# Kernel tuning notes

Hardware: AMD Instinct MI355X
Metric: run time of the kernel (lower is better)

Reference implementation:

```python
import jax, jax.numpy as jnp
import numpy as np

B, C, H, W, S = 4, 16, 256, 256, 100
OMEGA2 = (0.01 * S) ** 2  # alpha=0.01, n_spixels=100 -> 1.0
EPS = 1e-32


def setup_inputs() -> dict:
    key = jax.random.key(0)
    ks = jax.random.split(key, 7)
    pf = jax.random.normal(ks[0], (B, C, H, W), jnp.float32)
    spf1 = jax.random.normal(ks[1], (B, C, S), jnp.float32)
    spf2 = jax.random.normal(ks[2], (B, C, S), jnp.float32)
    Q1 = jax.random.uniform(ks[3], (B, S, H * W), jnp.float32)
    Q2 = jax.random.uniform(ks[4], (B, S, H * W), jnp.float32)
    w_ds = jax.random.normal(ks[5], (2, C, 3, 3), jnp.float32) * 0.05
    b_ds = jnp.zeros((2,), jnp.float32)
    return {"pf": pf, "spf1": spf1, "spf2": spf2, "Q1": Q1, "Q2": Q2,
            "w_ds": w_ds, "b_ds": b_ds}


def _affinity_pool(pf_flat, spf, Q):
    """merge=True branch: pairwise superpixel affinities, then affinity-weighted
    normalized pixel->superpixel pooling.
    pf_flat: [B,C,N], spf: [B,C,S] (detached), Q: [B,S,N] (detached)."""
    d = spf[:, :, None, :] - spf[:, :, :, None]          # [B,C,S,S]
    rels = jnp.exp(-jnp.sum(d * d, axis=1) / OMEGA2)      # [B,S,S]
    coeffs = jnp.einsum('bst,btn->bsn', rels, Q)          # map_sp2p(rels, Q)
    num = jnp.einsum('bcn,bsn->bcs', pf_flat, coeffs)     # pf @ coeffs^T
    return num / (jnp.sum(coeffs, axis=-1)[:, None, :] + EPS)  # [B,C,S]


def reference(pf, spf1, spf2, Q1, Q2, w_ds, b_ds):
    b, c, h, w = pf.shape
    pf_flat = pf.reshape(b, c, h * w)
    spf1n = _affinity_pool(pf_flat, spf1, Q1)
    spf2n = _affinity_pool(pf_flat, spf2, Q2)
    # map_sp2p: superpixel features back to pixels
    pf1 = jnp.einsum('bcs,bsn->bcn', spf1n, Q1).reshape(b, c, h, w)
    pf2 = jnp.einsum('bcs,bsn->bcn', spf2n, Q2).reshape(b, c, h, w)
    pf_sp = pf1 + pf2
    # conv_ds: Conv3x3(out_ch, 2), no bn/act
    prob_ds = jax.lax.conv_general_dilated(
        pf_sp, w_ds, window_strides=(1, 1), padding='SAME',
        dimension_numbers=('NCHW', 'OIHW', 'NCHW')) + b_ds[None, :, None, None]
    return prob_ds
```

## Files before the change

kernel.cpp:

```cpp
#include <hip/hip_runtime.h>

#define BB 4
#define CC 16
#define HH 256
#define WW 256
#define NN (HH*WW)
#define SS 100
#define SPL 5
#define EPSV 1e-32f

#define PQ_OFF    0u
#define SPFN_OFF  217600u
#define PFSP_OFF  230400u
#define PPART_OFF PFSP_OFF

__device__ __forceinline__ float dot4(const float4& a, const float4& b) {
    return a.x * b.x + a.y * b.y + a.z * b.z + a.w * b.w;
}
__device__ __forceinline__ void fma2g(float2& a, float c1, const float2& v1,
                                      float c2, const float2& v2) {
    a.x += c1 * v1.x + c2 * v2.x;
    a.y += c1 * v1.y + c2 * v2.y;
}

#define DPPQP(x, ctrl) __int_as_float(__builtin_amdgcn_update_dpp( \
    0, __float_as_int(x), ctrl, 0xF, 0xF, true))

__device__ __forceinline__ float dpp_sum64(float x) {
    #define DPPADD(ctrl) \
        x += __int_as_float(__builtin_amdgcn_update_dpp( \
            0, __float_as_int(x), ctrl, 0xF, 0xF, true));
    DPPADD(0x111)
    DPPADD(0x112)
    DPPADD(0x114)
    DPPADD(0x118)
    DPPADD(0x142)
    DPPADD(0x143)
    #undef DPPADD
    return x;
}

#define P1_LD0(k) (*(const float4*)(qptr + (size_t)(k) * NN))
#define P1_LD1(k) (*(const float4*)(qptr + (size_t)(k) * NN + 256))

#define P1_STEP(Q0, Q1, sidx) { \
    float t0 = dot4(p00,Q0)+dot4(p01,Q1), t1 = dot4(p10,Q0)+dot4(p11,Q1); \
    float t2 = dot4(p20,Q0)+dot4(p21,Q1), t3 = dot4(p30,Q0)+dot4(p31,Q1); \
    float t4 = dot4(p40,Q0)+dot4(p41,Q1), t5 = dot4(p50,Q0)+dot4(p51,Q1); \
    float t6 = dot4(p60,Q0)+dot4(p61,Q1), t7 = dot4(p70,Q0)+dot4(p71,Q1); \
    t0 += DPPQP(t0,0xB1); t1 += DPPQP(t1,0xB1); \
    t2 += DPPQP(t2,0xB1); t3 += DPPQP(t3,0xB1); \
    t4 += DPPQP(t4,0xB1); t5 += DPPQP(t5,0xB1); \
    t6 += DPPQP(t6,0xB1); t7 += DPPQP(t7,0xB1); \
    float u0 = odd ? t1 : t0; float u1 = odd ? t3 : t2; \
    float u2 = odd ? t5 : t4; float u3 = odd ? t7 : t6; \
    u0 += DPPQP(u0,0x4E); u1 += DPPQP(u1,0x4E); \
    u2 += DPPQP(u2,0x4E); u3 += DPPQP(u3,0x4E); \
    float w0 = hi2 ? u1 : u0; float w1 = hi2 ? u3 : u2; \
    w0 += DPPQP(w0,0x114); w1 += DPPQP(w1,0x114); \
    w0 += DPPQP(w0,0x118); w1 += DPPQP(w1,0x118); \
    w0 += __shfl_xor(w0,16); w1 += __shfl_xor(w1,16); \
    w0 += __shfl_xor(w0,32); w1 += __shfl_xor(w1,32); \
    float qv = Q0.x+Q0.y+Q0.z+Q0.w + Q1.x+Q1.y+Q1.z+Q1.w; \
    qv = dpp_sum64(qv); \
    if (h == 0 && lane == 63) sout[(size_t)(sidx)*17 + 16] = qv; \
    if (lane >= 12 && lane < 16) { \
        float* o = sout + (size_t)(sidx)*17 + h*8 + (lane-12); \
        o[0] = w0; o[4] = w1; \
    } \
}

__global__ __launch_bounds__(256, 4) void k_pass1(const float* __restrict__ pf,
                                                  const float* __restrict__ Q1,
                                                  const float* __restrict__ Q2,
                                                  float* __restrict__ ws) {
    int tid = threadIdx.x, wid = tid >> 6, lane = tid & 63;
    int h  = wid & 1;
    int nh = wid >> 1;
    int win = blockIdx.x;
    int sp  = blockIdx.y;
    int bq  = blockIdx.z;
    int b = bq >> 1, q = bq & 1;
    bool odd = lane & 1;
    bool hi2 = lane & 2;

    int nbase = win * 1024 + nh * 512 + lane * 4;
    const float* qptr = (q ? Q2 : Q1) + (size_t)b * SS * NN
                        + (size_t)(sp * 20) * NN + nbase;
    const float* PF   = pf + (size_t)b * CC * NN + (size_t)(h * 8) * NN + nbase;

    float4 p00 = *(const float4*)(PF + (size_t)0 * NN);
    float4 p01 = *(const float4*)(PF + (size_t)0 * NN + 256);
    float4 p10 = *(const float4*)(PF + (size_t)1 * NN);
    float4 p11 = *(const float4*)(PF + (size_t)1 * NN + 256);
    float4 p20 = *(const float4*)(PF + (size_t)2 * NN);
    float4 p21 = *(const float4*)(PF + (size_t)2 * NN + 256);
    float4 p30 = *(const float4*)(PF + (size_t)3 * NN);
    float4 p31 = *(const float4*)(PF + (size_t)3 * NN + 256);
    float4 p40 = *(const float4*)(PF + (size_t)4 * NN);
    float4 p41 = *(const float4*)(PF + (size_t)4 * NN + 256);
    float4 p50 = *(const float4*)(PF + (size_t)5 * NN);
    float4 p51 = *(const float4*)(PF + (size_t)5 * NN + 256);
    float4 p60 = *(const float4*)(PF + (size_t)6 * NN);
    float4 p61 = *(const float4*)(PF + (size_t)6 * NN + 256);
    float4 p70 = *(const float4*)(PF + (size_t)7 * NN);
    float4 p71 = *(const float4*)(PF + (size_t)7 * NN + 256);

    float* sout = ws + PPART_OFF
                + (size_t)((((bq * 64 + win) * 2 + nh) * SPL) + sp) * (20 * 17);

    float4 A0 = P1_LD0(0), A1 = P1_LD1(0), B0, B1;
    for (int s = 0; s < 17; s += 2) {
        B0 = P1_LD0(s + 1); B1 = P1_LD1(s + 1);
        P1_STEP(A0, A1, s)
        A0 = P1_LD0(s + 2); A1 = P1_LD1(s + 2);
        P1_STEP(B0, B1, s + 1)
    }
    B0 = P1_LD0(19); B1 = P1_LD1(19);
    P1_STEP(A0, A1, 18)
    P1_STEP(B0, B1, 19)
}

__global__ __launch_bounds__(256) void k_reduceP(float* __restrict__ ws) {
    int wg = blockIdx.x;
    int bq = blockIdx.y;
    int tid = threadIdx.x;
    const float* pp = ws + PPART_OFF + (size_t)(bq * 128 + wg * 16) * 1700;
    float a0 = 0.f, a1 = 0.f, a2 = 0.f, a3 = 0.f, a4 = 0.f, a5 = 0.f, a6 = 0.f;
    for (int wv = 0; wv < 16; ++wv) {
        const float* p = pp + (size_t)wv * 1700;
        a0 += p[tid];
        a1 += p[256 + tid];
        a2 += p[512 + tid];
        a3 += p[768 + tid];
        a4 += p[1024 + tid];
        a5 += p[1280 + tid];
        a6 += (1536 + tid < 1700) ? p[1536 + tid] : 0.f;
    }
    float* o = ws + PQ_OFF + (size_t)(bq * 8 + wg) * 1700;
    o[tid] = a0; o[256 + tid] = a1; o[512 + tid] = a2; o[768 + tid] = a3;
    o[1024 + tid] = a4; o[1280 + tid] = a5;
    if (1536 + tid < 1700) o[1536 + tid] = a6;
}

__global__ __launch_bounds__(256) void k_finalize(const float* __restrict__ spf1,
                                                  const float* __restrict__ spf2,
                                                  float* __restrict__ ws) {
    int bq = blockIdx.x;
    int b = bq >> 1, q = bq & 1;
    __shared__ float sp[CC][SS];
    __shared__ float rl[SS][SS + 1];
    __shared__ float Pl[CC * SS];
    __shared__ float qs[SS];
    __shared__ float den[SS];
    int tid = threadIdx.x;

    const float* spf = (q ? spf2 : spf1) + (size_t)b * CC * SS;
    for (int i = tid; i < CC * SS; i += 256) sp[i / SS][i % SS] = spf[i];
    __syncthreads();
    for (int i = tid; i < SS * SS; i += 256) {
        int s = i / SS, t = i % SS;
        float d2 = 0.f;
        #pragma unroll
        for (int c = 0; c < CC; ++c) {
            float d = sp[c][t] - sp[c][s];
            d2 += d * d;
        }
        rl[s][t] = expf(-d2);
    }
    const float* pq = ws + PQ_OFF + (size_t)bq * 8 * 1700;
    for (int idx = tid; idx < CC * SS; idx += 256) {
        int c = idx / SS, s = idx % SS;
        int slot = (s / 20) * 340 + (s % 20) * 17 + c;
        float v = 0.f;
        #pragma unroll 4
        for (int g = 0; g < 8; ++g) v += pq[(size_t)g * 1700 + slot];
        Pl[idx] = v;
    }
    if (tid < SS) {
        int slot = (tid / 20) * 340 + (tid % 20) * 17 + 16;
        float v = 0.f;
        #pragma unroll 4
        for (int g = 0; g < 8; ++g) v += pq[(size_t)g * 1700 + slot];
        qs[tid] = v;
    }
    __syncthreads();
    if (tid < SS) {
        float a = 0.f;
        for (int t = 0; t < SS; ++t) a += rl[tid][t] * qs[t];
        den[tid] = a + EPSV;
    }
    __syncthreads();
    float* sout = ws + SPFN_OFF + (size_t)bq * CC * SS;
    for (int idx = tid; idx < CC * SS; idx += 256) {
        int c = idx / SS, s = idx % SS;
        float a = 0.f;
        for (int t = 0; t < SS; ++t) a += rl[s][t] * Pl[c * SS + t];
        sout[idx] = a / den[s];
    }
}

#define P2FMA(X, s) { \
    _Pragma("unroll") for (int g = 0; g < 4; ++g) { \
        float4 s1 = *(const float4*)&sp[0][s][g * 4]; \
        float4 s2 = *(const float4*)&sp[1][s][g * 4]; \
        fma2g(acc[g*4+0], s1.x, X##1, s2.x, X##2); \
        fma2g(acc[g*4+1], s1.y, X##1, s2.y, X##2); \
        fma2g(acc[g*4+2], s1.z, X##1, s2.z, X##2); \
        fma2g(acc[g*4+3], s1.w, X##1, s2.w, X##2); } }

__global__ __launch_bounds__(128) void k_pass2(const float* __restrict__ Q1,
                                               const float* __restrict__ Q2,
                                               float* __restrict__ ws) {
    int blk = blockIdx.x;
    int b   = blockIdx.y;
    __shared__ float sp[2][SS][CC];
    int tid = threadIdx.x;
    const float* spin = ws + SPFN_OFF + (size_t)b * 2 * CC * SS;
    for (int idx = tid; idx < 2 * CC * SS; idx += 128) {
        int qq = idx / (CC * SS), rem = idx % (CC * SS);
        int c = rem / SS, s = rem % SS;
        sp[qq][s][c] = spin[idx];
    }
    __syncthreads();
    int n = blk * 256 + tid * 2;
    const float* q1p = Q1 + (size_t)b * SS * NN + n;
    const float* q2p = Q2 + (size_t)b * SS * NN + n;
    float2 acc[CC];
    #pragma unroll
    for (int c = 0; c < CC; ++c) acc[c] = make_float2(0.f, 0.f);
    float2 A1, A2, B1, B2;
    A1 = *(const float2*)(q1p);
    A2 = *(const float2*)(q2p);
    #pragma unroll 2
    for (int s = 0; s < 98; s += 2) {
        B1 = *(const float2*)(q1p + (size_t)(s + 1) * NN);
        B2 = *(const float2*)(q2p + (size_t)(s + 1) * NN);
        P2FMA(A, s)
        A1 = *(const float2*)(q1p + (size_t)(s + 2) * NN);
        A2 = *(const float2*)(q2p + (size_t)(s + 2) * NN);
        P2FMA(B, s + 1)
    }
    B1 = *(const float2*)(q1p + (size_t)99 * NN);
    B2 = *(const float2*)(q2p + (size_t)99 * NN);
    P2FMA(A, 98)
    P2FMA(B, 99)
    float* o = ws + PFSP_OFF + (size_t)b * CC * NN + n;
    #pragma unroll
    for (int c = 0; c < CC; ++c)
        *(float2*)(o + (size_t)c * NN) = acc[c];
}

__global__ __launch_bounds__(256) void k_conv(const float* __restrict__ w_ds,
                                              const float* __restrict__ b_ds,
                                              const float* __restrict__ ws,
                                              float* __restrict__ out) {
    int b = blockIdx.y;
    int n = blockIdx.x * 256 + threadIdx.x;
    __shared__ float wl[2][CC][9];
    __shared__ float bl[2];
    for (int i = threadIdx.x; i < 2 * CC * 9; i += 256)
        ((float*)wl)[i] = w_ds[i];
    if (threadIdx.x < 2) bl[threadIdx.x] = b_ds[threadIdx.x];
    __syncthreads();
    int y = n >> 8, x = n & 255;
    const float* base = ws + PFSP_OFF + (size_t)b * CC * NN;
    float a0 = bl[0], a1 = bl[1];
    for (int c = 0; c < CC; ++c) {
        const float* pc = base + (size_t)c * NN;
        #pragma unroll
        for (int dy = -1; dy <= 1; ++dy) {
            int yy = y + dy;
            if (yy < 0 || yy >= HH) continue;
            #pragma unroll
            for (int dx = -1; dx <= 1; ++dx) {
                int xx = x + dx;
                if (xx < 0 || xx >= WW) continue;
                float v = pc[(size_t)yy * WW + xx];
                int k = (dy + 1) * 3 + (dx + 1);
                a0 += v * wl[0][c][k];
                a1 += v * wl[1][c][k];
            }
        }
    }
    out[((size_t)b * 2 + 0) * NN + n] = a0;
    out[((size_t)b * 2 + 1) * NN + n] = a1;
}

extern "C" void kernel_launch(void* const* d_in, const int* in_sizes, int n_in,
                              void* d_out, int out_size, void* d_ws, size_t ws_size,
                              hipStream_t stream) {
    const float* pf   = (const float*)d_in[0];
    const float* spf1 = (const float*)d_in[1];
    const float* spf2 = (const float*)d_in[2];
    const float* Q1   = (const float*)d_in[3];
    const float* Q2   = (const float*)d_in[4];
    const float* w_ds = (const float*)d_in[5];
    const float* b_ds = (const float*)d_in[6];
    float* ws  = (float*)d_ws;
    float* out = (float*)d_out;

    k_pass1<<<dim3(64, SPL, 8), 256, 0, stream>>>(pf, Q1, Q2, ws);
    k_reduceP<<<dim3(8, 8), 256, 0, stream>>>(ws);
    k_finalize<<<8, 256, 0, stream>>>(spf1, spf2, ws);
    k_pass2<<<dim3(NN / 256, BB), 128, 0, stream>>>(Q1, Q2, ws);
    k_conv<<<dim3(NN / 256, BB), 256, 0, stream>>>(w_ds, b_ds, ws, out);
}
```

Baseline: 160.0 us.

## Repartition pass1 so each wave covers 4 channels over 1024 pixels

Each wave in the pixel-by-superpixel pooling pass now handles 4 channels across a full 1024-pixel window instead of 8 channels across 512 pixels. This removes the cross-wave shuffle reductions and shrinks the partial-sum buffer. The q-sum is computed only by the h==0 waves, and the partials now have a [win][s][4 groups][17] layout. The reduce and finalize kernels are rewritten to match, summing 64 windows and then 4 lane groups. The cost is doubled Q traffic per channel group, since 4 waves reread the same Q rows, and occupancy is lowered to launch_bounds(256,2).

```diff
diff --git a/kernel.cpp b/kernel.cpp
--- a/kernel.cpp
+++ b/kernel.cpp
@@ -10,12 +10,15 @@
 #define EPSV 1e-32f
 
 #define PQ_OFF    0u
-#define SPFN_OFF  217600u
-#define PFSP_OFF  230400u
+#define SPFN_OFF  54400u
+#define PFSP_OFF  67200u
 #define PPART_OFF PFSP_OFF
 
 __device__ __forceinline__ float dot4(const float4& a, const float4& b) {
     return a.x * b.x + a.y * b.y + a.z * b.z + a.w * b.w;
+}
+__device__ __forceinline__ float sum4(const float4& a) {
+    return a.x + a.y + a.z + a.w;
 }
 __device__ __forceinline__ void fma2g(float2& a, float c1, const float2& v1,
                                       float c2, const float2& v2) {
@@ -26,121 +29,110 @@
 #define DPPQP(x, ctrl) __int_as_float(__builtin_amdgcn_update_dpp( \
     0, __float_as_int(x), ctrl, 0xF, 0xF, true))
 
-__device__ __forceinline__ float dpp_sum64(float x) {
-    #define DPPADD(ctrl) \
-        x += __int_as_float(__builtin_amdgcn_update_dpp( \
-            0, __float_as_int(x), ctrl, 0xF, 0xF, true));
-    DPPADD(0x111)
-    DPPADD(0x112)
-    DPPADD(0x114)
-    DPPADD(0x118)
-    DPPADD(0x142)
-    DPPADD(0x143)
-    #undef DPPADD
-    return x;
-}
-
-#define P1_LD0(k) (*(const float4*)(qptr + (size_t)(k) * NN))
-#define P1_LD1(k) (*(const float4*)(qptr + (size_t)(k) * NN + 256))
-
-#define P1_STEP(Q0, Q1, sidx) { \
-    float t0 = dot4(p00,Q0)+dot4(p01,Q1), t1 = dot4(p10,Q0)+dot4(p11,Q1); \
-    float t2 = dot4(p20,Q0)+dot4(p21,Q1), t3 = dot4(p30,Q0)+dot4(p31,Q1); \
-    float t4 = dot4(p40,Q0)+dot4(p41,Q1), t5 = dot4(p50,Q0)+dot4(p51,Q1); \
-    float t6 = dot4(p60,Q0)+dot4(p61,Q1), t7 = dot4(p70,Q0)+dot4(p71,Q1); \
+#define QLD(X, k) \
+    X##0 = *(const float4*)(qptr + (size_t)(k) * NN); \
+    X##1 = *(const float4*)(qptr + (size_t)(k) * NN + 256); \
+    X##2 = *(const float4*)(qptr + (size_t)(k) * NN + 512); \
+    X##3 = *(const float4*)(qptr + (size_t)(k) * NN + 768);
+
+#define P1_STEP(X, sidx) { \
+    float t0 = dot4(p00,X##0)+dot4(p01,X##1)+dot4(p02,X##2)+dot4(p03,X##3); \
+    float t1 = dot4(p10,X##0)+dot4(p11,X##1)+dot4(p12,X##2)+dot4(p13,X##3); \
+    float t2 = dot4(p20,X##0)+dot4(p21,X##1)+dot4(p22,X##2)+dot4(p23,X##3); \
+    float t3 = dot4(p30,X##0)+dot4(p31,X##1)+dot4(p32,X##2)+dot4(p33,X##3); \
     t0 += DPPQP(t0,0xB1); t1 += DPPQP(t1,0xB1); \
     t2 += DPPQP(t2,0xB1); t3 += DPPQP(t3,0xB1); \
-    t4 += DPPQP(t4,0xB1); t5 += DPPQP(t5,0xB1); \
-    t6 += DPPQP(t6,0xB1); t7 += DPPQP(t7,0xB1); \
-    float u0 = odd ? t1 : t0; float u1 = odd ? t3 : t2; \
-    float u2 = odd ? t5 : t4; float u3 = odd ? t7 : t6; \
+    float u0 = odd ? t1 : t0; \
+    float u1 = odd ? t3 : t2; \
     u0 += DPPQP(u0,0x4E); u1 += DPPQP(u1,0x4E); \
-    u2 += DPPQP(u2,0x4E); u3 += DPPQP(u3,0x4E); \
-    float w0 = hi2 ? u1 : u0; float w1 = hi2 ? u3 : u2; \
-    w0 += DPPQP(w0,0x114); w1 += DPPQP(w1,0x114); \
-    w0 += DPPQP(w0,0x118); w1 += DPPQP(w1,0x118); \
-    w0 += __shfl_xor(w0,16); w1 += __shfl_xor(w1,16); \
-    w0 += __shfl_xor(w0,32); w1 += __shfl_xor(w1,32); \
-    float qv = Q0.x+Q0.y+Q0.z+Q0.w + Q1.x+Q1.y+Q1.z+Q1.w; \
-    qv = dpp_sum64(qv); \
-    if (h == 0 && lane == 63) sout[(size_t)(sidx)*17 + 16] = qv; \
-    if (lane >= 12 && lane < 16) { \
-        float* o = sout + (size_t)(sidx)*17 + h*8 + (lane-12); \
-        o[0] = w0; o[4] = w1; \
+    float w = hi2 ? u1 : u0; \
+    w += DPPQP(w,0x114); \
+    w += DPPQP(w,0x118); \
+    if (h == 0) { \
+        float qv = sum4(X##0)+sum4(X##1)+sum4(X##2)+sum4(X##3); \
+        qv += DPPQP(qv,0xB1); qv += DPPQP(qv,0x4E); \
+        qv += DPPQP(qv,0x114); qv += DPPQP(qv,0x118); \
+        if ((lane & 15) == 15) \
+            sout[(size_t)(sidx) * 68 + (lane >> 4) * 17 + 16] = qv; \
     } \
-}
-
-__global__ __launch_bounds__(256, 4) void k_pass1(const float* __restrict__ pf,
+    if ((lane & 15) >= 12) \
+        sout[(size_t)(sidx) * 68 + (lane >> 4) * 17 + h4 + (lane & 3)] = w; \
+}
+
+__global__ __launch_bounds__(256, 2) void k_pass1(const float* __restrict__ pf,
                                                   const float* __restrict__ Q1,
                                                   const float* __restrict__ Q2,
                                                   float* __restrict__ ws) {
     int tid = threadIdx.x, wid = tid >> 6, lane = tid & 63;
-    int h  = wid & 1;
-    int nh = wid >> 1;
-    int win = blockIdx.x;
-    int sp  = blockIdx.y;
-    int bq  = blockIdx.z;
+    int W = blockIdx.x * 4 + wid;
+    int h  = W & 3;
+    int t1i = W >> 2;
+    int sp  = t1i % 5;
+    int t2i = t1i / 5;
+    int win = t2i & 63;
+    int bq  = t2i >> 6;
     int b = bq >> 1, q = bq & 1;
     bool odd = lane & 1;
     bool hi2 = lane & 2;
-
-    int nbase = win * 1024 + nh * 512 + lane * 4;
+    int h4 = h * 4;
+
+    int nbase = win * 1024 + lane * 4;
     const float* qptr = (q ? Q2 : Q1) + (size_t)b * SS * NN
                         + (size_t)(sp * 20) * NN + nbase;
-    const float* PF   = pf + (size_t)b * CC * NN + (size_t)(h * 8) * NN + nbase;
+    const float* PF   = pf + (size_t)b * CC * NN + (size_t)h4 * NN + nbase;
 
     float4 p00 = *(const float4*)(PF + (size_t)0 * NN);
     float4 p01 = *(const float4*)(PF + (size_t)0 * NN + 256);
+    float4 p02 = *(const float4*)(PF + (size_t)0 * NN + 512);
+    float4 p03 = *(const float4*)(PF + (size_t)0 * NN + 768);
     float4 p10 = *(const float4*)(PF + (size_t)1 * NN);
     float4 p11 = *(const float4*)(PF + (size_t)1 * NN + 256);
+    float4 p12 = *(const float4*)(PF + (size_t)1 * NN + 512);
+    float4 p13 = *(const float4*)(PF + (size_t)1 * NN + 768);
     float4 p20 = *(const float4*)(PF + (size_t)2 * NN);
     float4 p21 = *(const float4*)(PF + (size_t)2 * NN + 256);
+    float4 p22 = *(const float4*)(PF + (size_t)2 * NN + 512);
+    float4 p23 = *(const float4*)(PF + (size_t)2 * NN + 768);
     float4 p30 = *(const float4*)(PF + (size_t)3 * NN);
     float4 p31 = *(const float4*)(PF + (size_t)3 * NN + 256);
-    float4 p40 = *(const float4*)(PF + (size_t)4 * NN);
-    float4 p41 = *(const float4*)(PF + (size_t)4 * NN + 256);
-    float4 p50 = *(const float4*)(PF + (size_t)5 * NN);
-    float4 p51 = *(const float4*)(PF + (size_t)5 * NN + 256);
-    float4 p60 = *(const float4*)(PF + (size_t)6 * NN);
-    float4 p61 = *(const float4*)(PF + (size_t)6 * NN + 256);
-    float4 p70 = *(const float4*)(PF + (size_t)7 * NN);
-    float4 p71 = *(const float4*)(PF + (size_t)7 * NN + 256);
+    float4 p32 = *(const float4*)(PF + (size_t)3 * NN + 512);
+    float4 p33 = *(const float4*)(PF + (size_t)3 * NN + 768);
 
     float* sout = ws + PPART_OFF
-                + (size_t)((((bq * 64 + win) * 2 + nh) * SPL) + sp) * (20 * 17);
-
-    float4 A0 = P1_LD0(0), A1 = P1_LD1(0), B0, B1;
-    for (int s = 0; s < 17; s += 2) {
-        B0 = P1_LD0(s + 1); B1 = P1_LD1(s + 1);
-        P1_STEP(A0, A1, s)
-        A0 = P1_LD0(s + 2); A1 = P1_LD1(s + 2);
-        P1_STEP(B0, B1, s + 1)
-    }
-    B0 = P1_LD0(19); B1 = P1_LD1(19);
-    P1_STEP(A0, A1, 18)
-    P1_STEP(B0, B1, 19)
+                + (size_t)((bq * 64 + win) * 100 + sp * 20) * 68;
+
+    float4 A0, A1, A2, A3, B0, B1, B2, B3;
+    QLD(A, 0)
+    for (int s = 0; s < 18; s += 2) {
+        QLD(B, s + 1)
+        P1_STEP(A, s)
+        QLD(A, s + 2)
+        P1_STEP(B, s + 1)
+    }
+    QLD(B, 19)
+    P1_STEP(A, 18)
+    P1_STEP(B, 19)
 }
 
 __global__ __launch_bounds__(256) void k_reduceP(float* __restrict__ ws) {
-    int wg = blockIdx.x;
-    int bq = blockIdx.y;
+    int sgc = blockIdx.x;
+    int bq  = blockIdx.y;
     int tid = threadIdx.x;
-    const float* pp = ws + PPART_OFF + (size_t)(bq * 128 + wg * 16) * 1700;
-    float a0 = 0.f, a1 = 0.f, a2 = 0.f, a3 = 0.f, a4 = 0.f, a5 = 0.f, a6 = 0.f;
-    for (int wv = 0; wv < 16; ++wv) {
-        const float* p = pp + (size_t)wv * 1700;
-        a0 += p[tid];
-        a1 += p[256 + tid];
-        a2 += p[512 + tid];
-        a3 += p[768 + tid];
-        a4 += p[1024 + tid];
-        a5 += p[1280 + tid];
-        a6 += (1536 + tid < 1700) ? p[1536 + tid] : 0.f;
-    }
-    float* o = ws + PQ_OFF + (size_t)(bq * 8 + wg) * 1700;
-    o[tid] = a0; o[256 + tid] = a1; o[512 + tid] = a2; o[768 + tid] = a3;
-    o[1024 + tid] = a4; o[1280 + tid] = a5;
-    if (1536 + tid < 1700) o[1536 + tid] = a6;
+    for (int o = tid; o < 680; o += 256) {
+        int sl = o / 68, slot = o % 68;
+        int sg = sgc * 10 + sl;
+        const float* pp = ws + PPART_OFF + (size_t)(bq * 64) * 6800
+                        + (size_t)sg * 68 + slot;
+        float a0 = 0.f, a1 = 0.f, a2 = 0.f, a3 = 0.f;
+        #pragma unroll 4
+        for (int win = 0; win < 64; win += 4) {
+            a0 += pp[(size_t)(win + 0) * 6800];
+            a1 += pp[(size_t)(win + 1) * 6800];
+            a2 += pp[(size_t)(win + 2) * 6800];
+            a3 += pp[(size_t)(win + 3) * 6800];
+        }
+        ws[PQ_OFF + (size_t)(bq * 100 + sg) * 68 + slot] = (a0 + a1) + (a2 + a3);
+    }
 }
 
 __global__ __launch_bounds__(256) void k_finalize(const float* __restrict__ spf1,
@@ -168,21 +160,15 @@
         }
         rl[s][t] = expf(-d2);
     }
-    const float* pq = ws + PQ_OFF + (size_t)bq * 8 * 1700;
+    const float* pq = ws + PQ_OFF + (size_t)bq * 100 * 68;
     for (int idx = tid; idx < CC * SS; idx += 256) {
         int c = idx / SS, s = idx % SS;
-        int slot = (s / 20) * 340 + (s % 20) * 17 + c;
-        float v = 0.f;
-        #pragma unroll 4
-        for (int g = 0; g < 8; ++g) v += pq[(size_t)g * 1700 + slot];
-        Pl[idx] = v;
+        const float* p = pq + (size_t)s * 68 + c;
+        Pl[idx] = (p[0] + p[17]) + (p[34] + p[51]);
     }
     if (tid < SS) {
-        int slot = (tid / 20) * 340 + (tid % 20) * 17 + 16;
-        float v = 0.f;
-        #pragma unroll 4
-        for (int g = 0; g < 8; ++g) v += pq[(size_t)g * 1700 + slot];
-        qs[tid] = v;
+        const float* p = pq + (size_t)tid * 68 + 16;
+        qs[tid] = (p[0] + p[17]) + (p[34] + p[51]);
     }
     __syncthreads();
     if (tid < SS) {
@@ -300,8 +286,8 @@
     float* ws  = (float*)d_ws;
     float* out = (float*)d_out;
 
-    k_pass1<<<dim3(64, SPL, 8), 256, 0, stream>>>(pf, Q1, Q2, ws);
-    k_reduceP<<<dim3(8, 8), 256, 0, stream>>>(ws);
+    k_pass1<<<2560, 256, 0, stream>>>(pf, Q1, Q2, ws);
+    k_reduceP<<<dim3(10, 8), 256, 0, stream>>>(ws);
     k_finalize<<<8, 256, 0, stream>>>(spf1, spf2, ws);
     k_pass2<<<dim3(NN / 256, BB), 128, 0, stream>>>(Q1, Q2, ws);
     k_conv<<<dim3(NN / 256, BB), 256, 0, stream>>>(w_ds, b_ds, ws, out);
```

Result: slower. 184.3 us (+15.1%).
